# Kernel optimization log

Measured on AMD Instinct MI355X. Metric: run time of the kernel, lower is better.

## Reference

```python
import jax, jax.numpy as jnp
import numpy as np

VISION_TOKEN_TYPE = 1
B, L, D, FF = 2, 2048, 1024, 4096


def setup_inputs() -> dict:
    key = jax.random.key(0)
    ks = jax.random.split(key, 8)
    s_in = 1.0 / np.sqrt(D)
    s_ff = 1.0 / np.sqrt(FF)
    return {
        "hidden_states": jax.random.normal(ks[0], (B, L, D), dtype=jnp.float32),
        "token_type_ids": jax.random.randint(ks[1], (B, L), 0, 2, dtype=jnp.int64),
        "v_gate": jax.random.normal(ks[2], (FF, D), dtype=jnp.float32) * s_in,
        "v_up": jax.random.normal(ks[3], (FF, D), dtype=jnp.float32) * s_in,
        "v_down": jax.random.normal(ks[4], (D, FF), dtype=jnp.float32) * s_ff,
        "l_gate": jax.random.normal(ks[5], (FF, D), dtype=jnp.float32) * s_in,
        "l_up": jax.random.normal(ks[6], (FF, D), dtype=jnp.float32) * s_in,
        "l_down": jax.random.normal(ks[7], (D, FF), dtype=jnp.float32) * s_ff,
    }


def _swiglu_mlp(x, w_gate, w_up, w_down):
    # x: (B, L, D); torch Linear stores weight as (out, in) -> contract on last dim
    g = jax.nn.silu(jnp.einsum("bld,fd->blf", x, w_gate))
    u = jnp.einsum("bld,fd->blf", x, w_up)
    return jnp.einsum("blf,df->bld", g * u, w_down)


def _vision_mask(token_type_ids):
    # vision token iff this token AND the next token are vision type; last col False
    t = token_type_ids == VISION_TOKEN_TYPE
    inner = t[:, :-1] & t[:, 1:]
    return jnp.concatenate([inner, jnp.zeros((t.shape[0], 1), dtype=bool)], axis=1)


def reference(hidden_states, token_type_ids, v_gate, v_up, v_down, l_gate, l_up, l_down):
    vision_mask = _vision_mask(token_type_ids)  # (B, L) bool
    vis_out = _swiglu_mlp(hidden_states, v_gate, v_up, v_down)
    lang_out = _swiglu_mlp(hidden_states, l_gate, l_up, l_down)
    return jnp.where(vision_mask[:, :, None], vis_out, lang_out)
```

## Files before the change

kernel.cpp:

```cpp
#include <hip/hip_runtime.h>
#include <hip/hip_bf16.h>
#include <stdint.h>


#define TOKENS 4096
#define SEQ    2048
#define DIM    1024
#define FFDIM  4096
#define MAXPAD 4608

typedef __attribute__((ext_vector_type(8))) short bf16x8;
typedef __attribute__((ext_vector_type(4))) float f32x4;

#define GAS __attribute__((address_space(1)))
#define LAS __attribute__((address_space(3)))

__device__ inline unsigned short f2bf(float x) {
    union { float f; unsigned int u; } c; c.f = x;
    unsigned int r = c.u + 0x7FFFu + ((c.u >> 16) & 1u);
    return (unsigned short)(r >> 16);
}
__device__ inline float bf2f(unsigned short u) {
    union { unsigned int i; float f; } c; c.i = ((unsigned int)u) << 16;
    return c.f;
}

struct __align__(16) us8 { unsigned short v[8]; };

__global__ __launch_bounds__(1024) void scan_kernel(const int* __restrict__ tt,
                                                    int* __restrict__ src_of,
                                                    int* __restrict__ counts) {
    __shared__ int sc[1024];
    const int tid = threadIdx.x;
    for (int i = tid; i < MAXPAD; i += 1024) src_of[i] = -1;

    const int t0 = tid * 4;
    int v[4], cnt = 0;
#pragma unroll
    for (int j = 0; j < 4; ++j) {
        const int t = t0 + j;
        const int l = t & (SEQ - 1);
        int vis = 0;
        if (l < SEQ - 1) vis = (tt[t] == 1) & (tt[t + 1] == 1);
        v[j] = vis; cnt += vis;
    }
    sc[tid] = cnt;
    __syncthreads();
    for (int off = 1; off < 1024; off <<= 1) {
        const int val = sc[tid];
        const int add = (tid >= off) ? sc[tid - off] : 0;
        __syncthreads();
        sc[tid] = val + add;
        __syncthreads();
    }
    const int totalV = sc[1023];
    const int excl   = sc[tid] - cnt;
    const int padNv  = (totalV + 127) & ~127;
    int pv = excl;
    int pl = padNv + (t0 - excl);
#pragma unroll
    for (int j = 0; j < 4; ++j) {
        const int t = t0 + j;
        if (v[j]) src_of[pv++] = t; else src_of[pl++] = t;
    }
    if (tid == 0) {
        const int Nl = TOKENS - totalV;
        counts[0] = padNv;
        counts[1] = padNv + ((Nl + 127) & ~127);
    }
}

__global__ void gather_cast(const float* __restrict__ hs, const int* __restrict__ src_of,
                            unsigned short* __restrict__ Xg) {
    const int gid = blockIdx.x * 256 + threadIdx.x;
    const int row = gid >> 7;
    const int c   = (gid & 127) * 8;
    const int src = src_of[row];
    us8 o;
    if (src >= 0) {
        const float4 a = *reinterpret_cast<const float4*>(hs + (size_t)src * DIM + c);
        const float4 b = *reinterpret_cast<const float4*>(hs + (size_t)src * DIM + c + 4);
        o.v[0] = f2bf(a.x); o.v[1] = f2bf(a.y); o.v[2] = f2bf(a.z); o.v[3] = f2bf(a.w);
        o.v[4] = f2bf(b.x); o.v[5] = f2bf(b.y); o.v[6] = f2bf(b.z); o.v[7] = f2bf(b.w);
    } else {
#pragma unroll
        for (int j = 0; j < 8; ++j) o.v[j] = 0;
    }
    *reinterpret_cast<us8*>(Xg + (size_t)row * DIM + c) = o;
}

__device__ inline void cast8(const float* __restrict__ in, unsigned short* __restrict__ out, int i) {
    const float4 a = *reinterpret_cast<const float4*>(in + i);
    const float4 b = *reinterpret_cast<const float4*>(in + i + 4);
    us8 o;
    o.v[0] = f2bf(a.x); o.v[1] = f2bf(a.y); o.v[2] = f2bf(a.z); o.v[3] = f2bf(a.w);
    o.v[4] = f2bf(b.x); o.v[5] = f2bf(b.y); o.v[6] = f2bf(b.z); o.v[7] = f2bf(b.w);
    *reinterpret_cast<us8*>(out + i) = o;
}

__global__ void cast6_kernel(const float* __restrict__ s0, const float* __restrict__ s1,
                             const float* __restrict__ s2, const float* __restrict__ s3,
                             const float* __restrict__ s4, const float* __restrict__ s5,
                             unsigned short* __restrict__ d0, unsigned short* __restrict__ d1,
                             unsigned short* __restrict__ d2, unsigned short* __restrict__ d3,
                             unsigned short* __restrict__ d4, unsigned short* __restrict__ d5) {
    const int i = (blockIdx.x * 256 + threadIdx.x) * 8;
    const int m = blockIdx.y;
    const float* s = (m == 0) ? s0 : (m == 1) ? s1 : (m == 2) ? s2 : (m == 3) ? s3 : (m == 4) ? s4 : s5;
    unsigned short* d = (m == 0) ? d0 : (m == 1) ? d1 : (m == 2) ? d2 : (m == 3) ? d3 : (m == 4) ? d4 : d5;
    cast8(s, d, i);
}

__global__ void cast4_kernel(const float* __restrict__ s0, const float* __restrict__ s1,
                             const float* __restrict__ s2, const float* __restrict__ s3,
                             unsigned short* __restrict__ d0, unsigned short* __restrict__ d1,
                             unsigned short* __restrict__ d2, unsigned short* __restrict__ d3) {
    const int i = (blockIdx.x * 256 + threadIdx.x) * 8;
    const int m = blockIdx.y;
    const float* s = (m == 0) ? s0 : (m == 1) ? s1 : (m == 2) ? s2 : s3;
    unsigned short* d = (m == 0) ? d0 : (m == 1) ? d1 : (m == 2) ? d2 : d3;
    cast8(s, d, i);
}

__global__ void cast2_kernel(const float* __restrict__ s0, const float* __restrict__ s1,
                             unsigned short* __restrict__ d0, unsigned short* __restrict__ d1) {
    const int i = (blockIdx.x * 256 + threadIdx.x) * 8;
    const float* s = blockIdx.y ? s1 : s0;
    unsigned short* d = blockIdx.y ? d1 : d0;
    cast8(s, d, i);
}

__global__ __launch_bounds__(256, 2) void gemm_p1(
    const unsigned short* __restrict__ A,
    const unsigned short* __restrict__ B0_v, const unsigned short* __restrict__ B1_v,
    const unsigned short* __restrict__ B0_l, const unsigned short* __restrict__ B1_l,
    unsigned short* __restrict__ H,
    const int* __restrict__ counts)
{
    __shared__ unsigned short Ls[256 * 64];

    const int m0 = blockIdx.y * 128;
    const int padNv = counts[0], padTot = counts[1];
    if (m0 >= padTot) return;
    const int expert = (m0 >= padNv);
    const unsigned short* B0 = expert ? B0_l : B0_v;
    const unsigned short* B1 = expert ? B1_l : B1_v;

    const int tid  = threadIdx.x;
    const int wid  = tid >> 6;
    const int lane = tid & 63;
    const int n0   = blockIdx.x * 64;

    constexpr int NI = 8;
    const unsigned short* src[NI];
    int loff[NI];
    const int cs = ((lane & 7) ^ (lane >> 3)) * 8;
#pragma unroll
    for (int i = 0; i < NI; ++i) {
        const int g = wid * 64 + i * 8 + (lane >> 3);
        const unsigned short* p;
        if (g < 128) {
            p = A + (size_t)(m0 + g) * DIM;
        } else {
            const int br = g - 128;
            p = (br < 64) ? (B0 + (size_t)(n0 + br) * DIM) : (B1 + (size_t)(n0 + br - 64) * DIM);
        }
        src[i] = p + cs;
        loff[i] = (wid * 64 + i * 8) * 64;
    }

    const int rlo = lane & 15;
    const int sw7 = rlo & 7;

    f32x4 acc[2][8];
#pragma unroll
    for (int i = 0; i < 2; ++i)
#pragma unroll
        for (int j = 0; j < 8; ++j)
            acc[i][j] = (f32x4){0.f, 0.f, 0.f, 0.f};

    const int NKT = DIM / 64;
#pragma unroll 1
    for (int kt = 0; kt < NKT; ++kt) {
        if (kt) __syncthreads();
        const int c = kt * 64;
#pragma unroll
        for (int i = 0; i < NI; ++i)
            __builtin_amdgcn_global_load_lds((const GAS void*)(src[i] + c),
                                             (LAS void*)&Ls[loff[i]], 16, 0, 0);
        asm volatile("s_waitcnt vmcnt(0)" ::: "memory");
        __syncthreads();

#pragma unroll
        for (int kh = 0; kh < 2; ++kh) {
            const int kc    = (lane >> 4) + kh * 4;
            const int swoff = (kc ^ sw7) * 8;
            const bf16x8 af0 = *reinterpret_cast<const bf16x8*>(&Ls[(wid * 32 + rlo) * 64 + swoff]);
            const bf16x8 af1 = *reinterpret_cast<const bf16x8*>(&Ls[(wid * 32 + 16 + rlo) * 64 + swoff]);
#pragma unroll
            for (int n = 0; n < 8; ++n) {
                const bf16x8 bfr = *reinterpret_cast<const bf16x8*>(&Ls[(128 + n * 16 + rlo) * 64 + swoff]);
                acc[0][n] = __builtin_amdgcn_mfma_f32_16x16x32_bf16(af0, bfr, acc[0][n], 0, 0, 0);
                acc[1][n] = __builtin_amdgcn_mfma_f32_16x16x32_bf16(af1, bfr, acc[1][n], 0, 0, 0);
            }
        }
    }

    const int rbase = m0 + wid * 32 + ((lane >> 4) * 4);
    const int cin   = lane & 15;
#pragma unroll
    for (int fr = 0; fr < 2; ++fr)
#pragma unroll
        for (int reg = 0; reg < 4; ++reg) {
            const int row = rbase + fr * 16 + reg;
#pragma unroll
            for (int n = 0; n < 4; ++n) {
                const float g = acc[fr][n][reg];
                const float u = acc[fr][n + 4][reg];
                const float h = g / (1.0f + __expf(-g)) * u;
                H[(size_t)row * FFDIM + n0 + n * 16 + cin] = f2bf(h);
            }
        }
}

__global__ __launch_bounds__(256, 2) void gemm_p2(
    const unsigned short* __restrict__ A,
    const unsigned short* __restrict__ Bd_v, const unsigned short* __restrict__ Bd_l,
    unsigned short* __restrict__ P,
    const int* __restrict__ counts)
{
    __shared__ unsigned short Ls[2][256 * 64];

    const int m0 = blockIdx.y * 128;
    const int padNv = counts[0], padTot = counts[1];
    if (m0 >= padTot) return;
    const unsigned short* B0 = (m0 >= padNv) ? Bd_l : Bd_v;

    const int tid  = threadIdx.x;
    const int wid  = tid >> 6;
    const int lane = tid & 63;
    const int wr   = wid >> 1;
    const int wc   = wid & 1;
    const int n0   = blockIdx.x * 128;
    const int kbase = blockIdx.z * (FFDIM / 2);

    constexpr int NI = 8;
    const unsigned short* src[NI];
    int loff[NI];
    const int cs = ((lane & 7) ^ (lane >> 3)) * 8;
#pragma unroll
    for (int i = 0; i < NI; ++i) {
        const int g = wid * 64 + i * 8 + (lane >> 3);
        const unsigned short* p = (g < 128)
            ? A + (size_t)(m0 + g) * FFDIM
            : B0 + (size_t)(n0 + g - 128) * FFDIM;
        src[i] = p + kbase + cs;
        loff[i] = (wid * 64 + i * 8) * 64;
    }

#define STAGE2(buf, kkt) do { \
    const int _c = (kkt) * 64; \
    _Pragma("unroll") \
    for (int i = 0; i < NI; ++i) \
        __builtin_amdgcn_global_load_lds((const GAS void*)(src[i] + _c), \
                                         (LAS void*)&Ls[buf][loff[i]], 16, 0, 0); \
} while (0)

    const int rlo = lane & 15;
    const int sw7 = rlo & 7;

    f32x4 acc[4][4];
#pragma unroll
    for (int i = 0; i < 4; ++i)
#pragma unroll
        for (int j = 0; j < 4; ++j)
            acc[i][j] = (f32x4){0.f, 0.f, 0.f, 0.f};

    STAGE2(0, 0);

    const int NKT = (FFDIM / 2) / 64;
    bf16x8 af[4], bf[4];
#pragma unroll 1
    for (int kt = 0; kt < NKT; ++kt) {
        const int cur = kt & 1;

        asm volatile("" ::: "memory");
        __builtin_amdgcn_s_barrier();
        asm volatile("" ::: "memory");

        if (kt + 1 < NKT) {
            STAGE2(cur ^ 1, kt + 1);
            asm volatile("s_waitcnt vmcnt(8)" ::: "memory");
        } else {
            asm volatile("s_waitcnt vmcnt(0)" ::: "memory");
        }

        asm volatile("" ::: "memory");
        __builtin_amdgcn_s_barrier();
        asm volatile("" ::: "memory");

#pragma unroll
        for (int kh = 0; kh < 2; ++kh) {
            const int kc    = (lane >> 4) + kh * 4;
            const int swoff = (kc ^ sw7) * 8;
#pragma unroll
            for (int i = 0; i < 4; ++i)
                af[i] = *reinterpret_cast<const bf16x8*>(&Ls[cur][(wr * 64 + i * 16 + rlo) * 64 + swoff]);
#pragma unroll
            for (int j = 0; j < 4; ++j)
                bf[j] = *reinterpret_cast<const bf16x8*>(&Ls[cur][(128 + wc * 64 + j * 16 + rlo) * 64 + swoff]);

            __builtin_amdgcn_s_setprio(1);
#pragma unroll
            for (int i = 0; i < 4; ++i)
#pragma unroll
                for (int j = 0; j < 4; ++j)
                    acc[i][j] = __builtin_amdgcn_mfma_f32_16x16x32_bf16(af[i], bf[j], acc[i][j], 0, 0, 0);
            __builtin_amdgcn_s_setprio(0);
        }
    }
#undef STAGE2

    unsigned short* Pz = P + (size_t)blockIdx.z * MAXPAD * DIM;
    const int rbase = m0 + wr * 64 + ((lane >> 4) * 4);
    const int cin   = lane & 15;
#pragma unroll
    for (int i = 0; i < 4; ++i)
#pragma unroll
        for (int reg = 0; reg < 4; ++reg) {
            const int row = rbase + i * 16 + reg;
#pragma unroll
            for (int j = 0; j < 4; ++j)
                Pz[(size_t)row * DIM + n0 + wc * 64 + j * 16 + cin] = f2bf(acc[i][j][reg]);
        }
}

__global__ void reduce_kernel(const unsigned short* __restrict__ P,
                              const int* __restrict__ src_of,
                              float* __restrict__ O) {
    const int gid = blockIdx.x * 256 + threadIdx.x;
    const int row = gid >> 7;
    const int c   = (gid & 127) * 8;
    const int src = src_of[row];
    if (src < 0) return;
    const us8 a = *reinterpret_cast<const us8*>(P + (size_t)row * DIM + c);
    const us8 b = *reinterpret_cast<const us8*>(P + (size_t)(MAXPAD + row) * DIM + c);
    float4 o0, o1;
    o0.x = bf2f(a.v[0]) + bf2f(b.v[0]);
    o0.y = bf2f(a.v[1]) + bf2f(b.v[1]);
    o0.z = bf2f(a.v[2]) + bf2f(b.v[2]);
    o0.w = bf2f(a.v[3]) + bf2f(b.v[3]);
    o1.x = bf2f(a.v[4]) + bf2f(b.v[4]);
    o1.y = bf2f(a.v[5]) + bf2f(b.v[5]);
    o1.z = bf2f(a.v[6]) + bf2f(b.v[6]);
    o1.w = bf2f(a.v[7]) + bf2f(b.v[7]);
    float* dst = O + (size_t)src * DIM + c;
    *reinterpret_cast<float4*>(dst)     = o0;
    *reinterpret_cast<float4*>(dst + 4) = o1;
}

extern "C" void kernel_launch(void* const* d_in, const int* in_sizes, int n_in,
                              void* d_out, int out_size, void* d_ws, size_t ws_size,
                              hipStream_t stream) {
    const float* hs = (const float*)d_in[0];
    const int*   tt = (const int*)d_in[1];
    const float* w_vg = (const float*)d_in[2];
    const float* w_vu = (const float*)d_in[3];
    const float* w_vd = (const float*)d_in[4];
    const float* w_lg = (const float*)d_in[5];
    const float* w_lu = (const float*)d_in[6];
    const float* w_ld = (const float*)d_in[7];
    float* out = (float*)d_out;
    char* ws = (char*)d_ws;

    const size_t MATB = (size_t)FFDIM * DIM * 2;
    const size_t XGB  = (size_t)MAXPAD * DIM * 2;
    const size_t HSZ  = (size_t)MAXPAD * FFDIM * 2;
    const size_t PART = 2 * XGB;

    int* counts = (int*)ws;
    int* src_of = (int*)(ws + 64);
    unsigned short* Xg = (unsigned short*)(ws + 32768);

    const int NELEM = FFDIM * DIM;
    const size_t need_big = 32768 + XGB + 6 * MATB + HSZ;

    scan_kernel<<<1, 1024, 0, stream>>>(tt, src_of, counts);
    gather_cast<<<MAXPAD * 128 / 256, 256, 0, stream>>>(hs, src_of, Xg);

    if (ws_size >= need_big) {
        unsigned short* Wg_v = (unsigned short*)(ws + 32768 + XGB);
        unsigned short* Wu_v = (unsigned short*)(ws + 32768 + XGB + MATB);
        unsigned short* Wg_l = (unsigned short*)(ws + 32768 + XGB + MATB * 2);
        unsigned short* Wu_l = (unsigned short*)(ws + 32768 + XGB + MATB * 3);
        unsigned short* Wd_v = (unsigned short*)(ws + 32768 + XGB + MATB * 4);
        unsigned short* Wd_l = (unsigned short*)(ws + 32768 + XGB + MATB * 5);
        unsigned short* H    = (unsigned short*)(ws + 32768 + XGB + MATB * 6);
        unsigned short* Part = Wg_v;

        dim3 gc6(NELEM / 2048, 6);
        cast6_kernel<<<gc6, 256, 0, stream>>>(w_vg, w_vu, w_lg, w_lu, w_vd, w_ld,
                                              Wg_v, Wu_v, Wg_l, Wu_l, Wd_v, Wd_l);

        dim3 g1(FFDIM / 64, MAXPAD / 128);
        gemm_p1<<<g1, 256, 0, stream>>>(Xg, Wg_v, Wu_v, Wg_l, Wu_l, H, counts);

        dim3 g2(DIM / 128, MAXPAD / 128, 2);
        gemm_p2<<<g2, 256, 0, stream>>>(H, Wd_v, Wd_l, Part, counts);

        reduce_kernel<<<MAXPAD * 128 / 256, 256, 0, stream>>>(Part, src_of, out);
    } else {
        unsigned short* Wg_v = (unsigned short*)(ws + 32768 + XGB);
        unsigned short* Wu_v = (unsigned short*)(ws + 32768 + XGB + MATB);
        unsigned short* Wg_l = (unsigned short*)(ws + 32768 + XGB + MATB * 2);
        unsigned short* Wu_l = (unsigned short*)(ws + 32768 + XGB + MATB * 3);
        unsigned short* H    = (unsigned short*)(ws + 32768 + XGB + MATB * 4);
        unsigned short* Wd_v = (unsigned short*)(ws + 32768);
        unsigned short* Wd_l = (unsigned short*)(ws + 32768 + MATB);
        unsigned short* Part = (unsigned short*)(ws + 32768 + MATB * 2);

        dim3 gc4(NELEM / 2048, 4);
        cast4_kernel<<<gc4, 256, 0, stream>>>(w_vg, w_vu, w_lg, w_lu, Wg_v, Wu_v, Wg_l, Wu_l);

        dim3 g1(FFDIM / 64, MAXPAD / 128);
        gemm_p1<<<g1, 256, 0, stream>>>(Xg, Wg_v, Wu_v, Wg_l, Wu_l, H, counts);

        dim3 gc2(NELEM / 2048, 2);
        cast2_kernel<<<gc2, 256, 0, stream>>>(w_vd, w_ld, Wd_v, Wd_l);

        dim3 g2(DIM / 128, MAXPAD / 128, 2);
        gemm_p2<<<g2, 256, 0, stream>>>(H, Wd_v, Wd_l, Part, counts);

        reduce_kernel<<<MAXPAD * 128 / 256, 256, 0, stream>>>(Part, src_of, out);
    }
}
```

Baseline: 181.6 us.

## Double-buffer gate/up GEMM with 512 threads, larger N tile and staged loads

Rewrites the fused gate/up GEMM kernel to use 8 waves over a 128x128 output tile (gate and up each 128 wide), with double-buffered LDS and global-to-LDS loads for the next K-step issued while the current one computes. Gate and up MFMAs are split into two phases with barriers and s_setprio so loads of the up slice and the next A/gate slice overlap compute. This is meant to hide global load latency and improve operand reuse per block. It raises LDS use to 96KB per block and adds more barriers, which may limit occupancy.

```diff
diff --git a/kernel.cpp b/kernel.cpp
--- a/kernel.cpp
+++ b/kernel.cpp
@@ -130,95 +130,152 @@
     cast8(s, d, i);
 }
 
-__global__ __launch_bounds__(256, 2) void gemm_p1(
+__global__ __launch_bounds__(512, 2) void gemm_p1(
     const unsigned short* __restrict__ A,
     const unsigned short* __restrict__ B0_v, const unsigned short* __restrict__ B1_v,
     const unsigned short* __restrict__ B0_l, const unsigned short* __restrict__ B1_l,
     unsigned short* __restrict__ H,
     const int* __restrict__ counts)
 {
-    __shared__ unsigned short Ls[256 * 64];
+    __shared__ unsigned short Ls[2][384 * 64];
 
     const int m0 = blockIdx.y * 128;
     const int padNv = counts[0], padTot = counts[1];
     if (m0 >= padTot) return;
     const int expert = (m0 >= padNv);
-    const unsigned short* B0 = expert ? B0_l : B0_v;
-    const unsigned short* B1 = expert ? B1_l : B1_v;
+    const unsigned short* Wg = expert ? B0_l : B0_v;
+    const unsigned short* Wu = expert ? B1_l : B1_v;
 
     const int tid  = threadIdx.x;
     const int wid  = tid >> 6;
     const int lane = tid & 63;
-    const int n0   = blockIdx.x * 64;
-
-    constexpr int NI = 8;
-    const unsigned short* src[NI];
-    int loff[NI];
-    const int cs = ((lane & 7) ^ (lane >> 3)) * 8;
-#pragma unroll
-    for (int i = 0; i < NI; ++i) {
-        const int g = wid * 64 + i * 8 + (lane >> 3);
-        const unsigned short* p;
-        if (g < 128) {
-            p = A + (size_t)(m0 + g) * DIM;
-        } else {
-            const int br = g - 128;
-            p = (br < 64) ? (B0 + (size_t)(n0 + br) * DIM) : (B1 + (size_t)(n0 + br - 64) * DIM);
-        }
-        src[i] = p + cs;
-        loff[i] = (wid * 64 + i * 8) * 64;
-    }
+    const int wr   = wid >> 2;
+    const int wc   = wid & 3;
+    const int n0   = blockIdx.x * 128;
+
+    const int cs   = ((lane & 7) ^ (lane >> 3)) * 8;
+    const int grow = wid * 8 + (lane >> 3);
+
+    const unsigned short* pA0 = A  + (size_t)(m0 + grow) * DIM + cs;
+    const unsigned short* pA1 = A  + (size_t)(m0 + 64 + grow) * DIM + cs;
+    const unsigned short* pG0 = Wg + (size_t)(n0 + grow) * DIM + cs;
+    const unsigned short* pG1 = Wg + (size_t)(n0 + 64 + grow) * DIM + cs;
+    const unsigned short* pU0 = Wu + (size_t)(n0 + grow) * DIM + cs;
+    const unsigned short* pU1 = Wu + (size_t)(n0 + 64 + grow) * DIM + cs;
+
+    const int dA0 = (      wid * 8) * 64;
+    const int dA1 = ( 64 + wid * 8) * 64;
+    const int dG0 = (128 + wid * 8) * 64;
+    const int dG1 = (192 + wid * 8) * 64;
+    const int dU0 = (256 + wid * 8) * 64;
+    const int dU1 = (320 + wid * 8) * 64;
+
+#define GLD(p, L, d) __builtin_amdgcn_global_load_lds((const GAS void*)(p), (LAS void*)((L) + (d)), 16, 0, 0)
+#define ST_AG(L, ko) do { GLD(pA0 + (ko), L, dA0); GLD(pA1 + (ko), L, dA1); \
+                          GLD(pG0 + (ko), L, dG0); GLD(pG1 + (ko), L, dG1); } while (0)
+#define ST_U(L, ko)  do { GLD(pU0 + (ko), L, dU0); GLD(pU1 + (ko), L, dU1); } while (0)
+
+    unsigned short* L0 = &Ls[0][0];
+    unsigned short* L1 = &Ls[1][0];
+
+    f32x4 acc[4][4];
+#pragma unroll
+    for (int i = 0; i < 4; ++i)
+#pragma unroll
+        for (int j = 0; j < 4; ++j)
+            acc[i][j] = (f32x4){0.f, 0.f, 0.f, 0.f};
+
+    ST_AG(L0, 0);
+    ST_U (L0, 0);
+    ST_AG(L1, 64);
+    asm volatile("s_waitcnt vmcnt(4)" ::: "memory");
+    asm volatile("" ::: "memory");
+    __builtin_amdgcn_s_barrier();
+    asm volatile("" ::: "memory");
 
     const int rlo = lane & 15;
     const int sw7 = rlo & 7;
-
-    f32x4 acc[2][8];
-#pragma unroll
-    for (int i = 0; i < 2; ++i)
-#pragma unroll
-        for (int j = 0; j < 8; ++j)
-            acc[i][j] = (f32x4){0.f, 0.f, 0.f, 0.f};
+    bf16x8 af[4][2], bg[2][2], bu[2][2];
 
     const int NKT = DIM / 64;
-#pragma unroll 1
+#pragma unroll 2
     for (int kt = 0; kt < NKT; ++kt) {
-        if (kt) __syncthreads();
-        const int c = kt * 64;
-#pragma unroll
-        for (int i = 0; i < NI; ++i)
-            __builtin_amdgcn_global_load_lds((const GAS void*)(src[i] + c),
-                                             (LAS void*)&Ls[loff[i]], 16, 0, 0);
-        asm volatile("s_waitcnt vmcnt(0)" ::: "memory");
-        __syncthreads();
+        unsigned short* Lc = (kt & 1) ? L1 : L0;
+        unsigned short* Ln = (kt & 1) ? L0 : L1;
 
 #pragma unroll
         for (int kh = 0; kh < 2; ++kh) {
-            const int kc    = (lane >> 4) + kh * 4;
-            const int swoff = (kc ^ sw7) * 8;
-            const bf16x8 af0 = *reinterpret_cast<const bf16x8*>(&Ls[(wid * 32 + rlo) * 64 + swoff]);
-            const bf16x8 af1 = *reinterpret_cast<const bf16x8*>(&Ls[(wid * 32 + 16 + rlo) * 64 + swoff]);
-#pragma unroll
-            for (int n = 0; n < 8; ++n) {
-                const bf16x8 bfr = *reinterpret_cast<const bf16x8*>(&Ls[(128 + n * 16 + rlo) * 64 + swoff]);
-                acc[0][n] = __builtin_amdgcn_mfma_f32_16x16x32_bf16(af0, bfr, acc[0][n], 0, 0, 0);
-                acc[1][n] = __builtin_amdgcn_mfma_f32_16x16x32_bf16(af1, bfr, acc[1][n], 0, 0, 0);
-            }
-        }
-    }
-
-    const int rbase = m0 + wid * 32 + ((lane >> 4) * 4);
-    const int cin   = lane & 15;
-#pragma unroll
-    for (int fr = 0; fr < 2; ++fr)
+            const int swoff = (((lane >> 4) + kh * 4) ^ sw7) * 8;
+#pragma unroll
+            for (int i = 0; i < 4; ++i)
+                af[i][kh] = *reinterpret_cast<const bf16x8*>(&Lc[(wr * 64 + i * 16 + rlo) * 64 + swoff]);
+#pragma unroll
+            for (int j = 0; j < 2; ++j)
+                bg[j][kh] = *reinterpret_cast<const bf16x8*>(&Lc[(128 + wc * 32 + j * 16 + rlo) * 64 + swoff]);
+        }
+        if (kt + 1 < NKT) ST_U(Ln, (kt + 1) * 64);
+        asm volatile("" ::: "memory");
+        __builtin_amdgcn_s_barrier();
+        asm volatile("s_waitcnt lgkmcnt(0)" ::: "memory");
+        __builtin_amdgcn_s_setprio(1);
+#pragma unroll
+        for (int kh = 0; kh < 2; ++kh)
+#pragma unroll
+            for (int i = 0; i < 4; ++i)
+#pragma unroll
+                for (int j = 0; j < 2; ++j)
+                    acc[i][j] = __builtin_amdgcn_mfma_f32_16x16x32_bf16(af[i][kh], bg[j][kh], acc[i][j], 0, 0, 0);
+        __builtin_amdgcn_s_setprio(0);
+        asm volatile("" ::: "memory");
+        __builtin_amdgcn_s_barrier();
+        asm volatile("" ::: "memory");
+
+#pragma unroll
+        for (int kh = 0; kh < 2; ++kh) {
+            const int swoff = (((lane >> 4) + kh * 4) ^ sw7) * 8;
+#pragma unroll
+            for (int j = 0; j < 2; ++j)
+                bu[j][kh] = *reinterpret_cast<const bf16x8*>(&Lc[(256 + wc * 32 + j * 16 + rlo) * 64 + swoff]);
+        }
+        if (kt + 2 < NKT) {
+            ST_AG(Lc, (kt + 2) * 64);
+            asm volatile("s_waitcnt vmcnt(4)" ::: "memory");
+        } else {
+            asm volatile("s_waitcnt vmcnt(0)" ::: "memory");
+        }
+        asm volatile("" ::: "memory");
+        __builtin_amdgcn_s_barrier();
+        asm volatile("s_waitcnt lgkmcnt(0)" ::: "memory");
+        __builtin_amdgcn_s_setprio(1);
+#pragma unroll
+        for (int kh = 0; kh < 2; ++kh)
+#pragma unroll
+            for (int i = 0; i < 4; ++i)
+#pragma unroll
+                for (int j = 0; j < 2; ++j)
+                    acc[i][2 + j] = __builtin_amdgcn_mfma_f32_16x16x32_bf16(af[i][kh], bu[j][kh], acc[i][2 + j], 0, 0, 0);
+        __builtin_amdgcn_s_setprio(0);
+        asm volatile("" ::: "memory");
+        __builtin_amdgcn_s_barrier();
+        asm volatile("" ::: "memory");
+    }
+#undef ST_AG
+#undef ST_U
+#undef GLD
+
+    const int rbase = m0 + wr * 64 + ((lane >> 4) * 4);
+    const int cbase = n0 + wc * 32 + (lane & 15);
+#pragma unroll
+    for (int i = 0; i < 4; ++i)
 #pragma unroll
         for (int reg = 0; reg < 4; ++reg) {
-            const int row = rbase + fr * 16 + reg;
-#pragma unroll
-            for (int n = 0; n < 4; ++n) {
-                const float g = acc[fr][n][reg];
-                const float u = acc[fr][n + 4][reg];
+            const int row = rbase + i * 16 + reg;
+#pragma unroll
+            for (int j = 0; j < 2; ++j) {
+                const float g = acc[i][j][reg];
+                const float u = acc[i][2 + j][reg];
                 const float h = g / (1.0f + __expf(-g)) * u;
-                H[(size_t)row * FFDIM + n0 + n * 16 + cin] = f2bf(h);
+                H[(size_t)row * FFDIM + cbase + j * 16] = f2bf(h);
             }
         }
 }
@@ -376,7 +433,6 @@
     const size_t MATB = (size_t)FFDIM * DIM * 2;
     const size_t XGB  = (size_t)MAXPAD * DIM * 2;
     const size_t HSZ  = (size_t)MAXPAD * FFDIM * 2;
-    const size_t PART = 2 * XGB;
 
     int* counts = (int*)ws;
     int* src_of = (int*)(ws + 64);
@@ -402,8 +458,8 @@
         cast6_kernel<<<gc6, 256, 0, stream>>>(w_vg, w_vu, w_lg, w_lu, w_vd, w_ld,
                                               Wg_v, Wu_v, Wg_l, Wu_l, Wd_v, Wd_l);
 
-        dim3 g1(FFDIM / 64, MAXPAD / 128);
-        gemm_p1<<<g1, 256, 0, stream>>>(Xg, Wg_v, Wu_v, Wg_l, Wu_l, H, counts);
+        dim3 g1(FFDIM / 128, MAXPAD / 128);
+        gemm_p1<<<g1, 512, 0, stream>>>(Xg, Wg_v, Wu_v, Wg_l, Wu_l, H, counts);
 
         dim3 g2(DIM / 128, MAXPAD / 128, 2);
         gemm_p2<<<g2, 256, 0, stream>>>(H, Wd_v, Wd_l, Part, counts);
@@ -422,8 +478,8 @@
         dim3 gc4(NELEM / 2048, 4);
         cast4_kernel<<<gc4, 256, 0, stream>>>(w_vg, w_vu, w_lg, w_lu, Wg_v, Wu_v, Wg_l, Wu_l);
 
-        dim3 g1(FFDIM / 64, MAXPAD / 128);
-        gemm_p1<<<g1, 256, 0, stream>>>(Xg, Wg_v, Wu_v, Wg_l, Wu_l, H, counts);
+        dim3 g1(FFDIM / 128, MAXPAD / 128);
+        gemm_p1<<<g1, 512, 0, stream>>>(Xg, Wg_v, Wu_v, Wg_l, Wu_l, H, counts);
 
         dim3 gc2(NELEM / 2048, 2);
         cast2_kernel<<<gc2, 256, 0, stream>>>(w_vd, w_ld, Wd_v, Wd_l);
```

After: 192.0 us. +5.7%, slower.

## Rewrite gate/up GEMM with 256x128 tiles, double-buffered LDS and phased prefetch

Applied to the files above, without the earlier changes.

The fused gate/up GEMM moves from a 128x64 single-buffered tile (256 threads) to a 256x128 tile per 512-thread block with two LDS buffers. Global-to-LDS loads for tile t+2 are split into groups and issued between MFMA phases, with barriers and s_setprio around each MFMA burst so loads overlap compute instead of waiting at vmcnt(0) every K step. Expert padding is raised to 256 so each M tile stays within one expert. The larger tiles raise reuse per byte loaded, at the cost of 128KB of LDS per block, more registers and fewer blocks in the grid.

```diff
diff --git a/kernel.cpp b/kernel.cpp
--- a/kernel.cpp
+++ b/kernel.cpp
@@ -55,7 +55,7 @@
     }
     const int totalV = sc[1023];
     const int excl   = sc[tid] - cnt;
-    const int padNv  = (totalV + 127) & ~127;
+    const int padNv  = (totalV + 255) & ~255;
     int pv = excl;
     int pl = padNv + (t0 - excl);
 #pragma unroll
@@ -66,7 +66,7 @@
     if (tid == 0) {
         const int Nl = TOKENS - totalV;
         counts[0] = padNv;
-        counts[1] = padNv + ((Nl + 127) & ~127);
+        counts[1] = padNv + ((Nl + 255) & ~255);
     }
 }
 
@@ -130,97 +130,196 @@
     cast8(s, d, i);
 }
 
-__global__ __launch_bounds__(256, 2) void gemm_p1(
+__global__ __launch_bounds__(512, 2) void gemm_p1(
     const unsigned short* __restrict__ A,
     const unsigned short* __restrict__ B0_v, const unsigned short* __restrict__ B1_v,
     const unsigned short* __restrict__ B0_l, const unsigned short* __restrict__ B1_l,
     unsigned short* __restrict__ H,
     const int* __restrict__ counts)
 {
-    __shared__ unsigned short Ls[256 * 64];
-
-    const int m0 = blockIdx.y * 128;
+    __shared__ unsigned short Ls[2][512 * 64];
+
+    const int m0 = blockIdx.y * 256;
     const int padNv = counts[0], padTot = counts[1];
     if (m0 >= padTot) return;
     const int expert = (m0 >= padNv);
-    const unsigned short* B0 = expert ? B0_l : B0_v;
-    const unsigned short* B1 = expert ? B1_l : B1_v;
+    const unsigned short* Wg = expert ? B0_l : B0_v;
+    const unsigned short* Wu = expert ? B1_l : B1_v;
 
     const int tid  = threadIdx.x;
     const int wid  = tid >> 6;
     const int lane = tid & 63;
-    const int n0   = blockIdx.x * 64;
-
-    constexpr int NI = 8;
-    const unsigned short* src[NI];
-    int loff[NI];
-    const int cs = ((lane & 7) ^ (lane >> 3)) * 8;
-#pragma unroll
-    for (int i = 0; i < NI; ++i) {
-        const int g = wid * 64 + i * 8 + (lane >> 3);
-        const unsigned short* p;
-        if (g < 128) {
-            p = A + (size_t)(m0 + g) * DIM;
-        } else {
-            const int br = g - 128;
-            p = (br < 64) ? (B0 + (size_t)(n0 + br) * DIM) : (B1 + (size_t)(n0 + br - 64) * DIM);
-        }
-        src[i] = p + cs;
-        loff[i] = (wid * 64 + i * 8) * 64;
-    }
+    const int wr   = wid >> 2;
+    const int wc   = wid & 3;
+    const int n0   = blockIdx.x * 128;
+
+    const int cs   = ((lane & 7) ^ (lane >> 3)) * 8;
+    const int rsub = wid * 8 + (lane >> 3);
+
+    const unsigned short* pS[8];
+    pS[0] = A  + (size_t)(m0 +   0 + rsub) * DIM + cs;
+    pS[1] = A  + (size_t)(m0 +  64 + rsub) * DIM + cs;
+    pS[2] = A  + (size_t)(m0 + 128 + rsub) * DIM + cs;
+    pS[3] = A  + (size_t)(m0 + 192 + rsub) * DIM + cs;
+    pS[4] = Wg + (size_t)(n0 +   0 + rsub) * DIM + cs;
+    pS[5] = Wg + (size_t)(n0 +  64 + rsub) * DIM + cs;
+    pS[6] = Wu + (size_t)(n0 +   0 + rsub) * DIM + cs;
+    pS[7] = Wu + (size_t)(n0 +  64 + rsub) * DIM + cs;
+
+    const int dW = wid * 8 * 64;
+
+    unsigned short* L0 = &Ls[0][0];
+    unsigned short* L1 = &Ls[1][0];
+
+#define GLD1(g, Lc, ko) __builtin_amdgcn_global_load_lds( \
+        (const GAS void*)(pS[g] + (ko)), \
+        (LAS void*)&(Lc)[(g) * 64 * 64 + dW], 16, 0, 0)
+#define PHASE_BAR() do { asm volatile("" ::: "memory"); \
+        __builtin_amdgcn_s_barrier(); asm volatile("" ::: "memory"); } while (0)
+
+    f32x4 accg[2][4][2], accu[2][4][2];
+#pragma unroll
+    for (int h = 0; h < 2; ++h)
+#pragma unroll
+        for (int i = 0; i < 4; ++i)
+#pragma unroll
+            for (int j = 0; j < 2; ++j) {
+                accg[h][i][j] = (f32x4){0.f, 0.f, 0.f, 0.f};
+                accu[h][i][j] = (f32x4){0.f, 0.f, 0.f, 0.f};
+            }
+
+#pragma unroll
+    for (int g = 0; g < 8; ++g) GLD1(g, L0, 0);
+#pragma unroll
+    for (int g = 0; g < 8; ++g) GLD1(g, L1, 64);
+    asm volatile("s_waitcnt vmcnt(8)" ::: "memory");
+    PHASE_BAR();
 
     const int rlo = lane & 15;
     const int sw7 = rlo & 7;
-
-    f32x4 acc[2][8];
-#pragma unroll
-    for (int i = 0; i < 2; ++i)
-#pragma unroll
-        for (int j = 0; j < 8; ++j)
-            acc[i][j] = (f32x4){0.f, 0.f, 0.f, 0.f};
+    bf16x8 af_lo[4][2], af_hi[4][2], bg[2][2], bu[2][2];
 
     const int NKT = DIM / 64;
+
+#define TILE_BODY(Lc, t) do {                                                          \
+    const int ko2 = ((t) + 2) * 64;                                                    \
+    const bool pf = ((t) + 2) < NKT;                                                   \
+                                                          \
+    _Pragma("unroll")                                                                  \
+    for (int kh = 0; kh < 2; ++kh) {                                                   \
+        const int swoff = (((lane >> 4) + kh * 4) ^ sw7) * 8;                          \
+        _Pragma("unroll")                                                              \
+        for (int i = 0; i < 4; ++i)                                                    \
+            af_lo[i][kh] = *reinterpret_cast<const bf16x8*>(                           \
+                &(Lc)[(wr * 128 + i * 16 + rlo) * 64 + swoff]);                        \
+        _Pragma("unroll")                                                              \
+        for (int j = 0; j < 2; ++j)                                                    \
+            bg[j][kh] = *reinterpret_cast<const bf16x8*>(                              \
+                &(Lc)[(256 + wc * 32 + j * 16 + rlo) * 64 + swoff]);                   \
+    }                                                                                  \
+    PHASE_BAR();                                                                       \
+    asm volatile("s_waitcnt lgkmcnt(0)" ::: "memory");                                 \
+    __builtin_amdgcn_s_setprio(1);                                                     \
+    _Pragma("unroll")                                                                  \
+    for (int kh = 0; kh < 2; ++kh)                                                     \
+        _Pragma("unroll")                                                              \
+        for (int i = 0; i < 4; ++i)                                                    \
+            _Pragma("unroll")                                                          \
+            for (int j = 0; j < 2; ++j)                                                \
+                accg[0][i][j] = __builtin_amdgcn_mfma_f32_16x16x32_bf16(               \
+                    af_lo[i][kh], bg[j][kh], accg[0][i][j], 0, 0, 0);                  \
+    __builtin_amdgcn_s_setprio(0);                                                     \
+    PHASE_BAR();                                                                       \
+               \
+    _Pragma("unroll")                                                                  \
+    for (int kh = 0; kh < 2; ++kh) {                                                   \
+        const int swoff = (((lane >> 4) + kh * 4) ^ sw7) * 8;                          \
+        _Pragma("unroll")                                                              \
+        for (int i = 0; i < 4; ++i)                                                    \
+            af_hi[i][kh] = *reinterpret_cast<const bf16x8*>(                           \
+                &(Lc)[(wr * 128 + 64 + i * 16 + rlo) * 64 + swoff]);                   \
+    }                                                                                  \
+    if (pf) { GLD1(0, Lc, ko2); GLD1(1, Lc, ko2); GLD1(4, Lc, ko2); GLD1(5, Lc, ko2); }\
+    PHASE_BAR();                                                                       \
+    asm volatile("s_waitcnt lgkmcnt(0)" ::: "memory");                                 \
+    __builtin_amdgcn_s_setprio(1);                                                     \
+    _Pragma("unroll")                                                                  \
+    for (int kh = 0; kh < 2; ++kh)                                                     \
+        _Pragma("unroll")                                                              \
+        for (int i = 0; i < 4; ++i)                                                    \
+            _Pragma("unroll")                                                          \
+            for (int j = 0; j < 2; ++j)                                                \
+                accg[1][i][j] = __builtin_amdgcn_mfma_f32_16x16x32_bf16(               \
+                    af_hi[i][kh], bg[j][kh], accg[1][i][j], 0, 0, 0);                  \
+    __builtin_amdgcn_s_setprio(0);                                                     \
+    PHASE_BAR();                                                                       \
+                                           \
+    _Pragma("unroll")                                                                  \
+    for (int kh = 0; kh < 2; ++kh) {                                                   \
+        const int swoff = (((lane >> 4) + kh * 4) ^ sw7) * 8;                          \
+        _Pragma("unroll")                                                              \
+        for (int j = 0; j < 2; ++j)                                                    \
+            bu[j][kh] = *reinterpret_cast<const bf16x8*>(                              \
+                &(Lc)[(384 + wc * 32 + j * 16 + rlo) * 64 + swoff]);                   \
+    }                                                                                  \
+    if (pf) { GLD1(2, Lc, ko2); GLD1(3, Lc, ko2); }                                    \
+    PHASE_BAR();                                                                       \
+    asm volatile("s_waitcnt lgkmcnt(0)" ::: "memory");                                 \
+    __builtin_amdgcn_s_setprio(1);                                                     \
+    _Pragma("unroll")                                                                  \
+    for (int kh = 0; kh < 2; ++kh)                                                     \
+        _Pragma("unroll")                                                              \
+        for (int i = 0; i < 4; ++i)                                                    \
+            _Pragma("unroll")                                                          \
+            for (int j = 0; j < 2; ++j)                                                \
+                accu[1][i][j] = __builtin_amdgcn_mfma_f32_16x16x32_bf16(               \
+                    af_hi[i][kh], bu[j][kh], accu[1][i][j], 0, 0, 0);                  \
+    __builtin_amdgcn_s_setprio(0);                                                     \
+    PHASE_BAR();                                                                       \
+       \
+    if (pf) { GLD1(6, Lc, ko2); GLD1(7, Lc, ko2); }                                    \
+    PHASE_BAR();                                                                       \
+    __builtin_amdgcn_s_setprio(1);                                                     \
+    _Pragma("unroll")                                                                  \
+    for (int kh = 0; kh < 2; ++kh)                                                     \
+        _Pragma("unroll")                                                              \
+        for (int i = 0; i < 4; ++i)                                                    \
+            _Pragma("unroll")                                                          \
+            for (int j = 0; j < 2; ++j)                                                \
+                accu[0][i][j] = __builtin_amdgcn_mfma_f32_16x16x32_bf16(               \
+                    af_lo[i][kh], bu[j][kh], accu[0][i][j], 0, 0, 0);                  \
+    __builtin_amdgcn_s_setprio(0);                                                     \
+    if (pf) { asm volatile("s_waitcnt vmcnt(8)" ::: "memory"); }                       \
+    else    { asm volatile("s_waitcnt vmcnt(0)" ::: "memory"); }                       \
+    PHASE_BAR();                                                                       \
+} while (0)
+
 #pragma unroll 1
-    for (int kt = 0; kt < NKT; ++kt) {
-        if (kt) __syncthreads();
-        const int c = kt * 64;
-#pragma unroll
-        for (int i = 0; i < NI; ++i)
-            __builtin_amdgcn_global_load_lds((const GAS void*)(src[i] + c),
-                                             (LAS void*)&Ls[loff[i]], 16, 0, 0);
-        asm volatile("s_waitcnt vmcnt(0)" ::: "memory");
-        __syncthreads();
-
-#pragma unroll
-        for (int kh = 0; kh < 2; ++kh) {
-            const int kc    = (lane >> 4) + kh * 4;
-            const int swoff = (kc ^ sw7) * 8;
-            const bf16x8 af0 = *reinterpret_cast<const bf16x8*>(&Ls[(wid * 32 + rlo) * 64 + swoff]);
-            const bf16x8 af1 = *reinterpret_cast<const bf16x8*>(&Ls[(wid * 32 + 16 + rlo) * 64 + swoff]);
-#pragma unroll
-            for (int n = 0; n < 8; ++n) {
-                const bf16x8 bfr = *reinterpret_cast<const bf16x8*>(&Ls[(128 + n * 16 + rlo) * 64 + swoff]);
-                acc[0][n] = __builtin_amdgcn_mfma_f32_16x16x32_bf16(af0, bfr, acc[0][n], 0, 0, 0);
-                acc[1][n] = __builtin_amdgcn_mfma_f32_16x16x32_bf16(af1, bfr, acc[1][n], 0, 0, 0);
+    for (int t = 0; t < NKT; t += 2) {
+        TILE_BODY(L0, t);
+        TILE_BODY(L1, t + 1);
+    }
+#undef TILE_BODY
+#undef GLD1
+#undef PHASE_BAR
+
+    const int rb = m0 + wr * 128 + ((lane >> 4) * 4);
+    const int cb = n0 + wc * 32 + (lane & 15);
+#pragma unroll
+    for (int h = 0; h < 2; ++h)
+#pragma unroll
+        for (int i = 0; i < 4; ++i)
+#pragma unroll
+            for (int reg = 0; reg < 4; ++reg) {
+                const int row = rb + h * 64 + i * 16 + reg;
+#pragma unroll
+                for (int j = 0; j < 2; ++j) {
+                    const float g = accg[h][i][j][reg];
+                    const float u = accu[h][i][j][reg];
+                    const float hv = g / (1.0f + __expf(-g)) * u;
+                    H[(size_t)row * FFDIM + cb + j * 16] = f2bf(hv);
+                }
             }
-        }
-    }
-
-    const int rbase = m0 + wid * 32 + ((lane >> 4) * 4);
-    const int cin   = lane & 15;
-#pragma unroll
-    for (int fr = 0; fr < 2; ++fr)
-#pragma unroll
-        for (int reg = 0; reg < 4; ++reg) {
-            const int row = rbase + fr * 16 + reg;
-#pragma unroll
-            for (int n = 0; n < 4; ++n) {
-                const float g = acc[fr][n][reg];
-                const float u = acc[fr][n + 4][reg];
-                const float h = g / (1.0f + __expf(-g)) * u;
-                H[(size_t)row * FFDIM + n0 + n * 16 + cin] = f2bf(h);
-            }
-        }
 }
 
 __global__ __launch_bounds__(256, 2) void gemm_p2(
@@ -376,7 +475,6 @@
     const size_t MATB = (size_t)FFDIM * DIM * 2;
     const size_t XGB  = (size_t)MAXPAD * DIM * 2;
     const size_t HSZ  = (size_t)MAXPAD * FFDIM * 2;
-    const size_t PART = 2 * XGB;
 
     int* counts = (int*)ws;
     int* src_of = (int*)(ws + 64);
@@ -402,8 +500,8 @@
         cast6_kernel<<<gc6, 256, 0, stream>>>(w_vg, w_vu, w_lg, w_lu, w_vd, w_ld,
                                               Wg_v, Wu_v, Wg_l, Wu_l, Wd_v, Wd_l);
 
-        dim3 g1(FFDIM / 64, MAXPAD / 128);
-        gemm_p1<<<g1, 256, 0, stream>>>(Xg, Wg_v, Wu_v, Wg_l, Wu_l, H, counts);
+        dim3 g1(FFDIM / 128, MAXPAD / 256);
+        gemm_p1<<<g1, 512, 0, stream>>>(Xg, Wg_v, Wu_v, Wg_l, Wu_l, H, counts);
 
         dim3 g2(DIM / 128, MAXPAD / 128, 2);
         gemm_p2<<<g2, 256, 0, stream>>>(H, Wd_v, Wd_l, Part, counts);
@@ -422,8 +520,8 @@
         dim3 gc4(NELEM / 2048, 4);
         cast4_kernel<<<gc4, 256, 0, stream>>>(w_vg, w_vu, w_lg, w_lu, Wg_v, Wu_v, Wg_l, Wu_l);
 
-        dim3 g1(FFDIM / 64, MAXPAD / 128);
-        gemm_p1<<<g1, 256, 0, stream>>>(Xg, Wg_v, Wu_v, Wg_l, Wu_l, H, counts);
+        dim3 g1(FFDIM / 128, MAXPAD / 256);
+        gemm_p1<<<g1, 512, 0, stream>>>(Xg, Wg_v, Wu_v, Wg_l, Wu_l, H, counts);
 
         dim3 gc2(NELEM / 2048, 2);
         cast2_kernel<<<gc2, 256, 0, stream>>>(w_vd, w_ld, Wd_v, Wd_l);
```

Result: slower. 216.9 us (+19.4%).
